# Kernel tuning notes

Measured on AMD Instinct MI355X. Metric: run time of the kernel, lower is better.

Reference implementation:

```python
import jax, jax.numpy as jnp
import numpy as np

THRESHOLD = 0.5

# Per face-direction (z-, z+, y-, y+, x-, x+), the 4 quad-vertex grid offsets
# (dz, dy, dx) where a coordinate c-0.5 maps to grid index c and c+0.5 to c+1.
# Order matches the original torch code's v0..v3 exactly.
QUAD_OFFS = np.array([
    [[0,0,0],[0,0,1],[0,1,0],[0,1,1]],  # z- face
    [[1,0,0],[1,0,1],[1,1,0],[1,1,1]],  # z+ face
    [[1,0,0],[1,0,1],[0,0,0],[0,0,1]],  # y- face
    [[0,1,0],[0,1,1],[1,1,0],[1,1,1]],  # y+ face
    [[1,0,0],[0,0,0],[1,1,0],[0,1,0]],  # x- face
    [[0,0,1],[1,0,1],[0,1,1],[1,1,1]],  # x+ face
], dtype=np.int32)
# Each quad -> 2 triangles: (v0,v1,v2), (v1,v2,v3)
TRI_SEL = np.array([[0,1,2],[1,2,3]], dtype=np.int32)
FACE_OFFS = QUAD_OFFS[:, TRI_SEL, :]  # [6, 2, 3, 3]


def setup_inputs() -> dict:
    key = jax.random.key(0)
    voxel_probas = jax.random.uniform(key, (4, 32, 32, 32), dtype=jnp.float32)
    return {"voxel_probas": voxel_probas}


def reference(voxel_probas):
    thr = THRESHOLD
    N, C, H, W = voxel_probas.shape
    occ = voxel_probas > thr
    pad = jnp.pad(occ, ((0, 0), (1, 1), (1, 1), (1, 1)))  # boundary = unoccupied
    # neighbor occupancy in the 6 directions (z-, z+, y-, y+, x-, x+)
    nb = jnp.stack([
        pad[:, :-2, 1:-1, 1:-1], pad[:, 2:, 1:-1, 1:-1],
        pad[:, 1:-1, :-2, 1:-1], pad[:, 1:-1, 2:, 1:-1],
        pad[:, 1:-1, 1:-1, :-2], pad[:, 1:-1, 1:-1, 2:],
    ], axis=-1)  # [N,C,H,W,6]
    exposed = occ[..., None] & ~nb  # face emitted iff voxel occupied & neighbor empty

    # canonical grid vertex ids (replaces python dict dedup; vertices live on a
    # (C+1)x(H+1)x(W+1) half-integer grid)
    zz, yy, xx = jnp.meshgrid(jnp.arange(C), jnp.arange(H), jnp.arange(W), indexing='ij')
    base = jnp.stack([zz, yy, xx], axis=-1)  # [C,H,W,3]
    gc = base[:, :, :, None, None, None, :] + jnp.asarray(FACE_OFFS)[None, None, None]  # [C,H,W,6,2,3,3]
    vid_local = (gc[..., 0] * (H + 1) + gc[..., 1]) * (W + 1) + gc[..., 2]  # [C,H,W,6,2,3]
    Vg = (C + 1) * (H + 1) * (W + 1)
    batch_off = (jnp.arange(N, dtype=jnp.int32) * Vg).reshape(N, 1, 1, 1, 1, 1, 1)
    faces = (vid_local[None].astype(jnp.int32) + batch_off).reshape(-1, 3)  # [Fmax,3]
    face_mask = jnp.repeat(exposed[..., None], 2, axis=-1).reshape(-1)       # [Fmax]

    # full grid vertex positions per sample (z-0.5, y-0.5, x-0.5 style coords)
    gz, gy, gx = jnp.meshgrid(jnp.arange(C + 1), jnp.arange(H + 1), jnp.arange(W + 1), indexing='ij')
    grid_pos = jnp.stack([gz, gy, gx], axis=-1).reshape(-1, 3).astype(jnp.float32) - 0.5
    vertex_positions = jnp.tile(grid_pos, (N, 1))  # [N*Vg,3]

    # which grid vertices are actually referenced by a valid face
    used = (jnp.zeros(N * Vg, jnp.int32)
            .at[faces.reshape(-1)]
            .add(jnp.repeat(face_mask.astype(jnp.int32), 3)) > 0)
    vpos_masked = jnp.where(used[:, None], vertex_positions, 0.0)

    # undirected edge index, same construction/order as the original:
    # (v0,v1) for all faces, then (v1,v2), then (v0,v2), then all reversed
    fwd_edges = jnp.concatenate([faces[:, [0, 1]], faces[:, [1, 2]], faces[:, [0, 2]]], axis=0)
    edge_index = jnp.concatenate([fwd_edges, fwd_edges[:, ::-1]], axis=0).T  # [2, 6*Fmax]
    edge_mask = jnp.tile(face_mask, 6)

    vert_counts = used.reshape(N, Vg).sum(-1)
    face_counts = face_mask.reshape(N, -1).sum(-1)
    return (vert_counts, face_counts, vpos_masked, used, edge_index, faces, face_mask, edge_mask)
```

## Files before the change

### kernel.cpp

```cpp
#include <hip/hip_runtime.h>

#define VG     35937
#define NVOX   131072
#define NPAIR  393216
#define NF4    393216

#define O_VC   0
#define O_FC   4
#define O_VP   8
#define O_US   431252
#define O_EI   575000
#define O_FA   19449368
#define O_FM   24167960
#define O_EM   25740824

#define NQB    1536
#define BPB    141
#define NVB    (4 * BPB)
#define NPART  (NQB + NVB)

template <int MODE>
__global__ __launch_bounds__(256) void cubify_fused(
    const float* __restrict__ probas, float* __restrict__ out,
    float* __restrict__ ws) {
  __shared__ int wsum[4];
  int lane = threadIdx.x & 63, wid = threadIdx.x >> 6;
  int b = blockIdx.x;

  if (b < NQB) {
    int t = b * 256 + threadIdx.x;
    int v = t / 3;
    int fp = t - 3 * v;
    int x = v & 31, y = (v >> 5) & 31, z = (v >> 10) & 31, n = v >> 15;

    float m0 = 0.0f, m1 = 0.0f;
    if (probas[v] > 0.5f) {
      bool nm, np;
      if (fp == 0)      { nm = (z > 0)  && probas[v - 1024] > 0.5f;
                          np = (z < 31) && probas[v + 1024] > 0.5f; }
      else if (fp == 1) { nm = (y > 0)  && probas[v - 32]   > 0.5f;
                          np = (y < 31) && probas[v + 32]   > 0.5f; }
      else              { nm = (x > 0)  && probas[v - 1]    > 0.5f;
                          np = (x < 31) && probas[v + 1]    > 0.5f; }
      m0 = nm ? 0.0f : 1.0f;
      m1 = np ? 0.0f : 1.0f;
    }

    int base = n * VG + (z * 33 + y) * 33 + x;
    float c0 = (float)(base);        float c1 = (float)(base + 1);
    float c2 = (float)(base + 33);   float c3 = (float)(base + 34);
    float c4 = (float)(base + 1089); float c5 = (float)(base + 1090);
    float c6 = (float)(base + 1122); float c7 = (float)(base + 1123);

    float a0, a1, a2, a3, b0, b1, b2, b3;
    if (fp == 0)      { a0=c0; a1=c1; a2=c2; a3=c3;  b0=c4; b1=c5; b2=c6; b3=c7; }
    else if (fp == 1) { a0=c4; a1=c5; a2=c0; a3=c1;  b0=c2; b1=c3; b2=c6; b3=c7; }
    else              { a0=c4; a1=c0; a2=c6; a3=c2;  b0=c1; b1=c5; b2=c3; b3=c7; }

    float4 M  = make_float4(m0, m0, m1, m1);
    float4 A  = make_float4(a0, a1, b0, b1);
    float4 B  = make_float4(a1, a2, b1, b2);
    float4 Cc = make_float4(a2, a3, b2, b3);

    ((float4*)(out + O_FM))[t] = M;

    float4* em = (float4*)(out + O_EM);
    #pragma unroll
    for (int j = 0; j < 6; ++j) em[j * NF4 + t] = M;

    float4* ei = (float4*)(out + O_EI);
    ei[ 0 * NF4 + t] = A;  ei[ 1 * NF4 + t] = B;  ei[ 2 * NF4 + t] = A;
    ei[ 3 * NF4 + t] = B;  ei[ 4 * NF4 + t] = Cc; ei[ 5 * NF4 + t] = Cc;
    ei[ 6 * NF4 + t] = B;  ei[ 7 * NF4 + t] = Cc; ei[ 8 * NF4 + t] = Cc;
    ei[ 9 * NF4 + t] = A;  ei[10 * NF4 + t] = B;  ei[11 * NF4 + t] = A;

    float4* fa = (float4*)(out + O_FA + 12 * t);
    fa[0] = make_float4(a0, a1, a2, a1);
    fa[1] = make_float4(a2, a3, b0, b1);
    fa[2] = make_float4(b2, b1, b2, b3);

    int cnt = 2 * ((m0 > 0.0f) + (m1 > 0.0f));
    for (int d = 32; d > 0; d >>= 1) cnt += __shfl_down(cnt, d, 64);
    if (lane == 0) wsum[wid] = cnt;
    __syncthreads();
    if (threadIdx.x == 0) {
      float s = (float)(wsum[0] + wsum[1] + wsum[2] + wsum[3]);
      if (MODE == 0) ws[b] = s;
      else atomicAdd(&out[O_FC + n], s);
    }
  } else {
    int b2 = b - NQB;
    int n  = b2 / BPB;
    int li = (b2 - n * BPB) * 256 + threadIdx.x;
    int u = 0;
    if (li < VG) {
      int gz = li / 1089;
      int r  = li - gz * 1089;
      int gy = r / 33;
      int gx = r - gy * 33;
      bool any_occ = false, all_occ = true;
      #pragma unroll
      for (int dz = 0; dz < 2; ++dz)
        #pragma unroll
        for (int dy = 0; dy < 2; ++dy)
          #pragma unroll
          for (int dx = 0; dx < 2; ++dx) {
            int z = gz - dz, y = gy - dy, x = gx - dx;
            if (z >= 0 && z < 32 && y >= 0 && y < 32 && x >= 0 && x < 32) {
              bool o = probas[((n * 32 + z) * 32 + y) * 32 + x] > 0.5f;
              any_occ |= o; all_occ &= o;
            } else {
              all_occ = false;
            }
          }
      u = (any_occ && !all_occ) ? 1 : 0;

      int idx = n * VG + li;
      out[O_US + idx] = u ? 1.0f : 0.0f;
      float* vp = out + O_VP + 3 * idx;
      if (u) {
        vp[0] = (float)gz - 0.5f;
        vp[1] = (float)gy - 0.5f;
        vp[2] = (float)gx - 0.5f;
      } else {
        vp[0] = 0.0f; vp[1] = 0.0f; vp[2] = 0.0f;
      }
    }
    int cnt = u;
    for (int d = 32; d > 0; d >>= 1) cnt += __shfl_down(cnt, d, 64);
    if (lane == 0) wsum[wid] = cnt;
    __syncthreads();
    if (threadIdx.x == 0) {
      float s = (float)(wsum[0] + wsum[1] + wsum[2] + wsum[3]);
      if (MODE == 0) ws[NQB + b2] = s;
      else atomicAdd(&out[O_VC + n], s);
    }
  }
}

__global__ __launch_bounds__(512) void counts_reduce(
    const float* __restrict__ ws, float* __restrict__ out) {
  int w = threadIdx.x >> 6, lane = threadIdx.x & 63;
  float s = 0.0f;
  if (w < 4) {
    for (int i = lane; i < BPB; i += 64) s += ws[NQB + w * BPB + i];
  } else {
    int n = w - 4;
    for (int i = lane; i < 384; i += 64) s += ws[n * 384 + i];
  }
  for (int d = 32; d > 0; d >>= 1) s += __shfl_down(s, d, 64);
  if (lane == 0) out[w] = s;
}

extern "C" void kernel_launch(void* const* d_in, const int* in_sizes, int n_in,
                              void* d_out, int out_size, void* d_ws, size_t ws_size,
                              hipStream_t stream) {
  const float* probas = (const float*)d_in[0];
  float* out = (float*)d_out;
  float* ws = (float*)d_ws;
  if (ws != nullptr && ws_size >= NPART * sizeof(float)) {
    cubify_fused<0><<<NQB + NVB, 256, 0, stream>>>(probas, out, ws);
    counts_reduce<<<1, 512, 0, stream>>>(ws, out);
  } else {
    cubify_fused<1><<<NQB + NVB, 256, 0, stream>>>(probas, out, ws);
  }
}
```

Measured before the change: 148.5 us.

## Split output writes into per-array blocks for contiguous coalesced stores

Instead of each thread writing 20 strided float4 stores across many output arrays, the grid is split into block ranges that each write one contiguous chunk of a single output (face_mask, edge_mask, edge_index, faces). Each thread recomputes its mask or corner indices, so every wavefront issues fully contiguous stores. This should improve write coalescing and DRAM page locality, since the kernel is dominated by roughly 100MB of writes. The cost is redundant recomputation of masks and neighbor loads, plus a much larger grid.

```diff
diff --git a/kernel.cpp b/kernel.cpp
--- a/kernel.cpp
+++ b/kernel.cpp
@@ -1,8 +1,6 @@
 #include <hip/hip_runtime.h>
 
 #define VG     35937
-#define NVOX   131072
-#define NPAIR  393216
 #define NF4    393216
 
 #define O_VC   0
@@ -14,84 +12,76 @@
 #define O_FM   24167960
 #define O_EM   25740824
 
-#define NQB    1536
 #define BPB    141
 #define NVB    (4 * BPB)
+#define NFMB   1536
+#define NEMB   9216
+#define NEIB   18432
+#define NFAB   4608
+#define B_FM   NVB
+#define B_EM   (B_FM + NFMB)
+#define B_EI   (B_EM + NEMB)
+#define B_FA   (B_EI + NEIB)
+#define NBLK   (B_FA + NFAB)
+
+#define NQB    1536
 #define NPART  (NQB + NVB)
 
+__device__ __forceinline__ void pair_decode(unsigned t, int& v, int& fp) {
+  unsigned uv = t / 3u;
+  fp = (int)(t - 3u * uv);
+  v = (int)uv;
+}
+
+struct Corners { int a0,a1,a2,a3,b0,b1,b2,b3; };
+__device__ __forceinline__ Corners corner_offs(int fp) {
+  Corners c;
+  c.a0 = fp==0 ? 0    : 1089;
+  c.a1 = fp==0 ? 1    : (fp==1 ? 1090 : 0);
+  c.a2 = fp==0 ? 33   : (fp==1 ? 0    : 1122);
+  c.a3 = fp==0 ? 34   : (fp==1 ? 1    : 33);
+  c.b0 = fp==0 ? 1089 : (fp==1 ? 33   : 1);
+  c.b1 = fp==1 ? 34   : 1090;
+  c.b2 = fp==2 ? 34   : 1122;
+  c.b3 = 1123;
+  return c;
+}
+
+__device__ __forceinline__ float2 pair_mask(const float* __restrict__ probas,
+                                            int v, int fp) {
+  int x = v & 31, y = (v >> 5) & 31, z = (v >> 10) & 31;
+  float m0 = 0.0f, m1 = 0.0f;
+  if (probas[v] > 0.5f) {
+    bool nm, np;
+    if (fp == 0)      { nm = (z > 0)  && probas[v - 1024] > 0.5f;
+                        np = (z < 31) && probas[v + 1024] > 0.5f; }
+    else if (fp == 1) { nm = (y > 0)  && probas[v - 32]   > 0.5f;
+                        np = (y < 31) && probas[v + 32]   > 0.5f; }
+    else              { nm = (x > 0)  && probas[v - 1]    > 0.5f;
+                        np = (x < 31) && probas[v + 1]    > 0.5f; }
+    m0 = nm ? 0.0f : 1.0f;
+    m1 = np ? 0.0f : 1.0f;
+  }
+  return make_float2(m0, m1);
+}
+
+__device__ __forceinline__ int pair_base(int v) {
+  int x = v & 31, y = (v >> 5) & 31, z = (v >> 10) & 31, n = v >> 15;
+  return n * VG + (z * 33 + y) * 33 + x;
+}
+
 template <int MODE>
-__global__ __launch_bounds__(256) void cubify_fused(
+__global__ __launch_bounds__(256) void cubify_main(
     const float* __restrict__ probas, float* __restrict__ out,
     float* __restrict__ ws) {
   __shared__ int wsum[4];
-  int lane = threadIdx.x & 63, wid = threadIdx.x >> 6;
+  int tid = threadIdx.x;
+  int lane = tid & 63, wid = tid >> 6;
   int b = blockIdx.x;
 
-  if (b < NQB) {
-    int t = b * 256 + threadIdx.x;
-    int v = t / 3;
-    int fp = t - 3 * v;
-    int x = v & 31, y = (v >> 5) & 31, z = (v >> 10) & 31, n = v >> 15;
-
-    float m0 = 0.0f, m1 = 0.0f;
-    if (probas[v] > 0.5f) {
-      bool nm, np;
-      if (fp == 0)      { nm = (z > 0)  && probas[v - 1024] > 0.5f;
-                          np = (z < 31) && probas[v + 1024] > 0.5f; }
-      else if (fp == 1) { nm = (y > 0)  && probas[v - 32]   > 0.5f;
-                          np = (y < 31) && probas[v + 32]   > 0.5f; }
-      else              { nm = (x > 0)  && probas[v - 1]    > 0.5f;
-                          np = (x < 31) && probas[v + 1]    > 0.5f; }
-      m0 = nm ? 0.0f : 1.0f;
-      m1 = np ? 0.0f : 1.0f;
-    }
-
-    int base = n * VG + (z * 33 + y) * 33 + x;
-    float c0 = (float)(base);        float c1 = (float)(base + 1);
-    float c2 = (float)(base + 33);   float c3 = (float)(base + 34);
-    float c4 = (float)(base + 1089); float c5 = (float)(base + 1090);
-    float c6 = (float)(base + 1122); float c7 = (float)(base + 1123);
-
-    float a0, a1, a2, a3, b0, b1, b2, b3;
-    if (fp == 0)      { a0=c0; a1=c1; a2=c2; a3=c3;  b0=c4; b1=c5; b2=c6; b3=c7; }
-    else if (fp == 1) { a0=c4; a1=c5; a2=c0; a3=c1;  b0=c2; b1=c3; b2=c6; b3=c7; }
-    else              { a0=c4; a1=c0; a2=c6; a3=c2;  b0=c1; b1=c5; b2=c3; b3=c7; }
-
-    float4 M  = make_float4(m0, m0, m1, m1);
-    float4 A  = make_float4(a0, a1, b0, b1);
-    float4 B  = make_float4(a1, a2, b1, b2);
-    float4 Cc = make_float4(a2, a3, b2, b3);
-
-    ((float4*)(out + O_FM))[t] = M;
-
-    float4* em = (float4*)(out + O_EM);
-    #pragma unroll
-    for (int j = 0; j < 6; ++j) em[j * NF4 + t] = M;
-
-    float4* ei = (float4*)(out + O_EI);
-    ei[ 0 * NF4 + t] = A;  ei[ 1 * NF4 + t] = B;  ei[ 2 * NF4 + t] = A;
-    ei[ 3 * NF4 + t] = B;  ei[ 4 * NF4 + t] = Cc; ei[ 5 * NF4 + t] = Cc;
-    ei[ 6 * NF4 + t] = B;  ei[ 7 * NF4 + t] = Cc; ei[ 8 * NF4 + t] = Cc;
-    ei[ 9 * NF4 + t] = A;  ei[10 * NF4 + t] = B;  ei[11 * NF4 + t] = A;
-
-    float4* fa = (float4*)(out + O_FA + 12 * t);
-    fa[0] = make_float4(a0, a1, a2, a1);
-    fa[1] = make_float4(a2, a3, b0, b1);
-    fa[2] = make_float4(b2, b1, b2, b3);
-
-    int cnt = 2 * ((m0 > 0.0f) + (m1 > 0.0f));
-    for (int d = 32; d > 0; d >>= 1) cnt += __shfl_down(cnt, d, 64);
-    if (lane == 0) wsum[wid] = cnt;
-    __syncthreads();
-    if (threadIdx.x == 0) {
-      float s = (float)(wsum[0] + wsum[1] + wsum[2] + wsum[3]);
-      if (MODE == 0) ws[b] = s;
-      else atomicAdd(&out[O_FC + n], s);
-    }
-  } else {
-    int b2 = b - NQB;
-    int n  = b2 / BPB;
-    int li = (b2 - n * BPB) * 256 + threadIdx.x;
+  if (b < NVB) {
+    int n  = b / BPB;
+    int li = (b - n * BPB) * 256 + tid;
     int u = 0;
     if (li < VG) {
       int gz = li / 1089;
@@ -130,11 +120,68 @@
     for (int d = 32; d > 0; d >>= 1) cnt += __shfl_down(cnt, d, 64);
     if (lane == 0) wsum[wid] = cnt;
     __syncthreads();
-    if (threadIdx.x == 0) {
+    if (tid == 0) {
       float s = (float)(wsum[0] + wsum[1] + wsum[2] + wsum[3]);
-      if (MODE == 0) ws[NQB + b2] = s;
+      if (MODE == 0) ws[NQB + b] = s;
       else atomicAdd(&out[O_VC + n], s);
     }
+  } else if (b < B_EM) {
+    int qb = b - B_FM;
+    unsigned t = (unsigned)qb * 256u + tid;
+    int v, fp; pair_decode(t, v, fp);
+    float2 m = pair_mask(probas, v, fp);
+    ((float4*)(out + O_FM))[t] = make_float4(m.x, m.x, m.y, m.y);
+
+    int cnt = 2 * ((m.x > 0.0f) + (m.y > 0.0f));
+    for (int d = 32; d > 0; d >>= 1) cnt += __shfl_down(cnt, d, 64);
+    if (lane == 0) wsum[wid] = cnt;
+    __syncthreads();
+    if (tid == 0) {
+      float s = (float)(wsum[0] + wsum[1] + wsum[2] + wsum[3]);
+      if (MODE == 0) ws[qb] = s;
+      else atomicAdd(&out[O_FC + (v >> 15)], s);
+    }
+  } else if (b < B_EI) {
+    int e  = b - B_EM;
+    int ch = e / 1536;
+    unsigned t = (unsigned)(e - ch * 1536) * 256u + tid;
+    unsigned g = (unsigned)e * 256u + tid;
+    int v, fp; pair_decode(t, v, fp);
+    float2 m = pair_mask(probas, v, fp);
+    ((float4*)(out + O_EM))[g] = make_float4(m.x, m.x, m.y, m.y);
+  } else if (b < B_FA) {
+    int e  = b - B_EI;
+    int ch = e / 1536;
+    unsigned t = (unsigned)(e - ch * 1536) * 256u + tid;
+    unsigned g = (unsigned)e * 256u + tid;
+    int v, fp; pair_decode(t, v, fp);
+    int base = pair_base(v);
+    Corners c = corner_offs(fp);
+    const unsigned pat = (0u<<0)|(1u<<2)|(0u<<4)|(1u<<6)|(2u<<8)|(2u<<10)|
+                         (1u<<12)|(2u<<14)|(2u<<16)|(0u<<18)|(1u<<20)|(0u<<22);
+    int sel = (pat >> (2 * ch)) & 3;
+    float4 val;
+    if (sel == 0)       val = make_float4((float)(base + c.a0), (float)(base + c.a1),
+                                          (float)(base + c.b0), (float)(base + c.b1));
+    else if (sel == 1)  val = make_float4((float)(base + c.a1), (float)(base + c.a2),
+                                          (float)(base + c.b1), (float)(base + c.b2));
+    else                val = make_float4((float)(base + c.a2), (float)(base + c.a3),
+                                          (float)(base + c.b2), (float)(base + c.b3));
+    ((float4*)(out + O_EI))[g] = val;
+  } else {
+    int e = b - B_FA;
+    unsigned g = (unsigned)e * 256u + tid;
+    unsigned t = g / 3u;
+    int r = (int)(g - 3u * t);
+    int v, fp; pair_decode(t, v, fp);
+    int base = pair_base(v);
+    Corners c = corner_offs(fp);
+    int w0 = r==0 ? c.a0 : (r==1 ? c.a2 : c.b2);
+    int w1 = r==0 ? c.a1 : (r==1 ? c.a3 : c.b1);
+    int w2 = r==0 ? c.a2 : (r==1 ? c.b0 : c.b2);
+    int w3 = r==0 ? c.a1 : (r==1 ? c.b1 : c.b3);
+    ((float4*)(out + O_FA))[g] = make_float4((float)(base + w0), (float)(base + w1),
+                                             (float)(base + w2), (float)(base + w3));
   }
 }
 
@@ -159,9 +206,9 @@
   float* out = (float*)d_out;
   float* ws = (float*)d_ws;
   if (ws != nullptr && ws_size >= NPART * sizeof(float)) {
-    cubify_fused<0><<<NQB + NVB, 256, 0, stream>>>(probas, out, ws);
+    cubify_main<0><<<NBLK, 256, 0, stream>>>(probas, out, ws);
     counts_reduce<<<1, 512, 0, stream>>>(ws, out);
   } else {
-    cubify_fused<1><<<NQB + NVB, 256, 0, stream>>>(probas, out, ws);
-  }
-}
+    cubify_main<1><<<NBLK, 256, 0, stream>>>(probas, out, ws);
+  }
+}
```

Result: no change. 147.5 us (-0.7%).
